# Kernel tuning notes

Measured on AMD Instinct MI355X. Metric: run time of the kernel, lower is better.

## Reference

```python
import jax, jax.numpy as jnp
import numpy as np

IN_FEATURES = 4096
OUT_FEATURES = 11008
GROUP_SIZE = 128


def setup_inputs() -> dict:
    key = jax.random.key(0)
    k_x, k_w, k_s, k_z, k_b = jax.random.split(key, 5)
    x = jax.random.normal(k_x, (8, IN_FEATURES), dtype=jnp.float32)
    # packed INT4 weights: two 4-bit values per byte, stored in int32 (0..255)
    weight_q = jax.random.randint(k_w, (OUT_FEATURES, IN_FEATURES // 2), 0, 256, dtype=jnp.int32)
    num_groups = IN_FEATURES // GROUP_SIZE  # 32
    scales = jax.random.uniform(k_s, (OUT_FEATURES, num_groups), dtype=jnp.float32) * 0.01 + 1e-4
    zeros = jax.random.normal(k_z, (OUT_FEATURES, num_groups), dtype=jnp.float32) * 0.05
    bias = jax.random.normal(k_b, (OUT_FEATURES,), dtype=jnp.float32) * 0.02
    return {"x": x, "weight_q": weight_q, "scales": scales, "zeros": zeros, "bias": bias}


def _dequantize(weight_q, scales, zeros):
    # unpack INT4: low nibble first, then high nibble (matches torch stack order)
    low = weight_q & 15
    high = (weight_q >> 4) & 15
    q = jnp.stack([low, high], axis=-1).reshape(OUT_FEATURES, -1)  # [out, in]
    q = q.astype(scales.dtype)
    num_groups = scales.shape[1]
    q = q[:, : num_groups * GROUP_SIZE].reshape(OUT_FEATURES, num_groups, GROUP_SIZE)
    w = q * scales[:, :, None] + zeros[:, :, None]
    return w.reshape(OUT_FEATURES, -1)[:, :IN_FEATURES]


def reference(x, weight_q, scales, zeros, bias):
    w = _dequantize(weight_q, scales, zeros)            # [out, in]
    return x.astype(w.dtype) @ w.T + bias               # [B, out]
```

## Files before the change

### kernel.cpp

```cpp
#include <hip/hip_runtime.h>

typedef _Float16 f16;
typedef __attribute__((ext_vector_type(2))) _Float16 f16x2;
typedef __attribute__((ext_vector_type(4))) _Float16 f16x4;
typedef __attribute__((ext_vector_type(8))) _Float16 f16x8;
typedef __attribute__((ext_vector_type(4))) float f32x4;
typedef __attribute__((ext_vector_type(4))) unsigned u32x4;

constexpr int IN_F  = 4096;
constexpr int OUT_F = 11008;
constexpr int NGRP  = 32;

__global__ void xprep_kernel(const float* __restrict__ x, f16* __restrict__ xh) {
    int i = (blockIdx.x * blockDim.x + threadIdx.x) * 4;
    float4 v = *(const float4*)(x + i);
    f16x4 r = {(f16)v.x, (f16)v.y, (f16)v.z, (f16)v.w};
    *(f16x4*)(xh + i) = r;
}

__device__ __forceinline__ unsigned dq2(unsigned q, f16x2 sp, f16x2 zp) {
    unsigned t = (((q << 12) | q) & 0x000F000Fu) | 0x64006400u;
    f16x2 u = __builtin_bit_cast(f16x2, t);
    u = u - (f16x2){(_Float16)1024.0f, (_Float16)1024.0f};
    u = u * sp + zp;
    return __builtin_bit_cast(unsigned, u);
}

__device__ __forceinline__ f16x2 bcast(float v) {
    _Float16 h = (_Float16)v;
    return (f16x2){h, h};
}

template<bool PRE>
__global__ __launch_bounds__(256, 4)
void qlin_kernel(const int* __restrict__ wq,
                 const float* __restrict__ scales,
                 const float* __restrict__ zeros,
                 const float* __restrict__ bias,
                 const float* __restrict__ xf,
                 const f16* __restrict__ xh,
                 float* __restrict__ out)
{
    __shared__ f32x4 red[4][64];
    const int tid  = threadIdx.x;
    const int wv   = tid >> 6;
    const int lane = tid & 63;
    const int col  = lane & 15;
    const int kg   = lane >> 4;
    const int o0   = blockIdx.x * 16;
    const int orow = o0 + col;
    const bool mvalid = (col < 8);

    const int kbase = wv * 1024;
    const int g0    = kbase >> 7;

    float4 sa = *(const float4*)(scales + (size_t)orow * NGRP + g0);
    float4 sb = *(const float4*)(scales + (size_t)orow * NGRP + g0 + 4);
    float4 za = *(const float4*)(zeros  + (size_t)orow * NGRP + g0);
    float4 zb = *(const float4*)(zeros  + (size_t)orow * NGRP + g0 + 4);
    f16x2 sp[8] = {bcast(sa.x), bcast(sa.y), bcast(sa.z), bcast(sa.w),
                   bcast(sb.x), bcast(sb.y), bcast(sb.z), bcast(sb.w)};
    f16x2 zp[8] = {bcast(za.x), bcast(za.y), bcast(za.z), bcast(za.w),
                   bcast(zb.x), bcast(zb.y), bcast(zb.z), bcast(zb.w)};

    const int*   wbase = wq + (size_t)orow * (IN_F / 2) + (kbase >> 1) + kg * 4;
    const f16*   xrow  = xh + (size_t)col * IN_F + kbase + kg * 8;
    const float* xfrow = xf + (size_t)col * IN_F + kbase + kg * 8;

    f32x4 acc = {0.f, 0.f, 0.f, 0.f};

    int4  qb[2][4];
    f16x8 ab[2][4];

    #pragma unroll
    for (int t = 0; t < 4; ++t) {
        qb[0][t] = *(const int4*)(wbase + t * 16);
        if (mvalid) {
            if constexpr (PRE) {
                ab[0][t] = *(const f16x8*)(xrow + t * 32);
            } else {
                float4 a0 = *(const float4*)(xfrow + t * 32);
                float4 a1 = *(const float4*)(xfrow + t * 32 + 4);
                ab[0][t] = (f16x8){(f16)a0.x,(f16)a0.y,(f16)a0.z,(f16)a0.w,
                                   (f16)a1.x,(f16)a1.y,(f16)a1.z,(f16)a1.w};
            }
        } else {
            ab[0][t] = (f16x8){0,0,0,0,0,0,0,0};
        }
    }

    #pragma unroll
    for (int gl = 0; gl < 8; ++gl) {
        const int cur = gl & 1, nxt = cur ^ 1;
        if (gl < 7) {
            #pragma unroll
            for (int t = 0; t < 4; ++t) {
                qb[nxt][t] = *(const int4*)(wbase + (gl + 1) * 64 + t * 16);
                if (mvalid) {
                    if constexpr (PRE) {
                        ab[nxt][t] = *(const f16x8*)(xrow + (gl + 1) * 128 + t * 32);
                    } else {
                        float4 a0 = *(const float4*)(xfrow + (gl + 1) * 128 + t * 32);
                        float4 a1 = *(const float4*)(xfrow + (gl + 1) * 128 + t * 32 + 4);
                        ab[nxt][t] = (f16x8){(f16)a0.x,(f16)a0.y,(f16)a0.z,(f16)a0.w,
                                             (f16)a1.x,(f16)a1.y,(f16)a1.z,(f16)a1.w};
                    }
                } else {
                    ab[nxt][t] = (f16x8){0,0,0,0,0,0,0,0};
                }
            }
        }
        const f16x2 s2 = sp[gl], z2 = zp[gl];
        #pragma unroll
        for (int t = 0; t < 4; ++t) {
            const int4 q = qb[cur][t];
            u32x4 bw = {dq2((unsigned)q.x, s2, z2),
                        dq2((unsigned)q.y, s2, z2),
                        dq2((unsigned)q.z, s2, z2),
                        dq2((unsigned)q.w, s2, z2)};
            f16x8 bfr = __builtin_bit_cast(f16x8, bw);
            acc = __builtin_amdgcn_mfma_f32_16x16x32_f16(ab[cur][t], bfr, acc, 0, 0, 0);
        }
    }

    red[wv][lane] = acc;
    __syncthreads();

    if (tid < 64) {
        f32x4 ssum = red[0][tid];
        #pragma unroll
        for (int w = 1; w < 4; ++w) ssum += red[w][tid];
        const int n = tid & 15;
        const float bb = bias[o0 + n];
        const int mbase = (tid >> 4) * 4;
        if (mbase < 8) {
            #pragma unroll
            for (int i = 0; i < 4; ++i)
                out[(size_t)(mbase + i) * OUT_F + o0 + n] = ssum[i] + bb;
        }
    }
}

extern "C" void kernel_launch(void* const* d_in, const int* in_sizes, int n_in,
                              void* d_out, int out_size, void* d_ws, size_t ws_size,
                              hipStream_t stream) {
    const float* x  = (const float*)d_in[0];
    const int*   wq = (const int*)d_in[1];
    const float* sc = (const float*)d_in[2];
    const float* zr = (const float*)d_in[3];
    const float* bs = (const float*)d_in[4];
    float* out = (float*)d_out;

    if (ws_size >= (size_t)(8 * IN_F * sizeof(f16))) {
        f16* xh = (f16*)d_ws;
        xprep_kernel<<<(8 * IN_F) / (256 * 4), 256, 0, stream>>>(x, xh);
        qlin_kernel<true><<<OUT_F / 16, 256, 0, stream>>>(wq, sc, zr, bs, x, xh, out);
    } else {
        qlin_kernel<false><<<OUT_F / 16, 256, 0, stream>>>(wq, sc, zr, bs, x, (const f16*)d_ws, out);
    }
}
```

Measured before the change: 31.11 us.

## Stage INT4 weight tiles into LDS via direct global-to-LDS async loads

Replaces per-lane register prefetch of packed weights with a double-buffered LDS staging scheme that uses global_load_lds, where each wave loads whole contiguous 1 KB row slices with an XOR swizzle. It also re-partitions K so that waves interleave over 128-element chunks within each 512-wide stage, and loads scales and zeros as scalar gathers. The aim is fully coalesced weight streaming and better latency hiding. In exchange it adds 32 KB of LDS per block, which limits occupancy, and a __syncthreads per stage.

```diff
diff --git a/kernel.cpp b/kernel.cpp
--- a/kernel.cpp
+++ b/kernel.cpp
@@ -41,7 +41,9 @@
                  const f16* __restrict__ xh,
                  float* __restrict__ out)
 {
+    __shared__ unsigned char wlds[2][16][1024];
     __shared__ f32x4 red[4][64];
+
     const int tid  = threadIdx.x;
     const int wv   = tid >> 6;
     const int lane = tid & 63;
@@ -51,76 +53,75 @@
     const int orow = o0 + col;
     const bool mvalid = (col < 8);
 
-    const int kbase = wv * 1024;
-    const int g0    = kbase >> 7;
+    f16x2 sp[8], zp[8];
+    #pragma unroll
+    for (int s = 0; s < 8; ++s) {
+        sp[s] = bcast(scales[(size_t)orow * NGRP + s * 4 + wv]);
+        zp[s] = bcast(zeros [(size_t)orow * NGRP + s * 4 + wv]);
+    }
 
-    float4 sa = *(const float4*)(scales + (size_t)orow * NGRP + g0);
-    float4 sb = *(const float4*)(scales + (size_t)orow * NGRP + g0 + 4);
-    float4 za = *(const float4*)(zeros  + (size_t)orow * NGRP + g0);
-    float4 zb = *(const float4*)(zeros  + (size_t)orow * NGRP + g0 + 4);
-    f16x2 sp[8] = {bcast(sa.x), bcast(sa.y), bcast(sa.z), bcast(sa.w),
-                   bcast(sb.x), bcast(sb.y), bcast(sb.z), bcast(sb.w)};
-    f16x2 zp[8] = {bcast(za.x), bcast(za.y), bcast(za.z), bcast(za.w),
-                   bcast(zb.x), bcast(zb.y), bcast(zb.z), bcast(zb.w)};
+    const char* wtile = (const char*)wq + (size_t)o0 * 8192;
 
-    const int*   wbase = wq + (size_t)orow * (IN_F / 2) + (kbase >> 1) + kg * 4;
-    const f16*   xrow  = xh + (size_t)col * IN_F + kbase + kg * 8;
-    const float* xfrow = xf + (size_t)col * IN_F + kbase + kg * 8;
+    auto stage = [&](int sl, int bufi) {
+        #pragma unroll
+        for (int c = 0; c < 4; ++c) {
+            const int r = 4 * wv + c;
+            const char* src = wtile + (size_t)r * 8192 + sl * 1024
+                              + ((lane * 16) ^ ((r & 7) << 4));
+            __builtin_amdgcn_global_load_lds(
+                (const __attribute__((address_space(1))) void*)src,
+                (__attribute__((address_space(3))) void*)&wlds[bufi][r][0],
+                16, 0, 0);
+        }
+    };
+
+    stage(0, 0);
+
+    const f16*   xcol  = xh + (size_t)col * IN_F;
+    const float* xfcol = xf + (size_t)col * IN_F;
+    const unsigned swz = (unsigned)((col & 7) << 4);
 
     f32x4 acc = {0.f, 0.f, 0.f, 0.f};
 
-    int4  qb[2][4];
-    f16x8 ab[2][4];
+    __syncthreads();
 
     #pragma unroll
-    for (int t = 0; t < 4; ++t) {
-        qb[0][t] = *(const int4*)(wbase + t * 16);
-        if (mvalid) {
-            if constexpr (PRE) {
-                ab[0][t] = *(const f16x8*)(xrow + t * 32);
+    for (int s = 0; s < 8; ++s) {
+        const int cur = s & 1;
+        if (s < 7) stage(s + 1, cur ^ 1);
+
+        f16x8 af[4];
+        #pragma unroll
+        for (int t = 0; t < 4; ++t) {
+            const int k = s * 512 + wv * 128 + t * 32 + kg * 8;
+            if (mvalid) {
+                if constexpr (PRE) {
+                    af[t] = *(const f16x8*)(xcol + k);
+                } else {
+                    float4 a0 = *(const float4*)(xfcol + k);
+                    float4 a1 = *(const float4*)(xfcol + k + 4);
+                    af[t] = (f16x8){(f16)a0.x,(f16)a0.y,(f16)a0.z,(f16)a0.w,
+                                    (f16)a1.x,(f16)a1.y,(f16)a1.z,(f16)a1.w};
+                }
             } else {
-                float4 a0 = *(const float4*)(xfrow + t * 32);
-                float4 a1 = *(const float4*)(xfrow + t * 32 + 4);
-                ab[0][t] = (f16x8){(f16)a0.x,(f16)a0.y,(f16)a0.z,(f16)a0.w,
-                                   (f16)a1.x,(f16)a1.y,(f16)a1.z,(f16)a1.w};
-            }
-        } else {
-            ab[0][t] = (f16x8){0,0,0,0,0,0,0,0};
-        }
-    }
-
-    #pragma unroll
-    for (int gl = 0; gl < 8; ++gl) {
-        const int cur = gl & 1, nxt = cur ^ 1;
-        if (gl < 7) {
-            #pragma unroll
-            for (int t = 0; t < 4; ++t) {
-                qb[nxt][t] = *(const int4*)(wbase + (gl + 1) * 64 + t * 16);
-                if (mvalid) {
-                    if constexpr (PRE) {
-                        ab[nxt][t] = *(const f16x8*)(xrow + (gl + 1) * 128 + t * 32);
-                    } else {
-                        float4 a0 = *(const float4*)(xfrow + (gl + 1) * 128 + t * 32);
-                        float4 a1 = *(const float4*)(xfrow + (gl + 1) * 128 + t * 32 + 4);
-                        ab[nxt][t] = (f16x8){(f16)a0.x,(f16)a0.y,(f16)a0.z,(f16)a0.w,
-                                             (f16)a1.x,(f16)a1.y,(f16)a1.z,(f16)a1.w};
-                    }
-                } else {
-                    ab[nxt][t] = (f16x8){0,0,0,0,0,0,0,0};
-                }
+                af[t] = (f16x8){0,0,0,0,0,0,0,0};
             }
         }
-        const f16x2 s2 = sp[gl], z2 = zp[gl];
+
+        const f16x2 s2 = sp[s], z2 = zp[s];
         #pragma unroll
         for (int t = 0; t < 4; ++t) {
-            const int4 q = qb[cur][t];
+            const unsigned off = ((unsigned)(wv * 256 + t * 64 + kg * 16)) ^ swz;
+            const int4 q = *(const int4*)&wlds[cur][col][off];
             u32x4 bw = {dq2((unsigned)q.x, s2, z2),
                         dq2((unsigned)q.y, s2, z2),
                         dq2((unsigned)q.z, s2, z2),
                         dq2((unsigned)q.w, s2, z2)};
             f16x8 bfr = __builtin_bit_cast(f16x8, bw);
-            acc = __builtin_amdgcn_mfma_f32_16x16x32_f16(ab[cur][t], bfr, acc, 0, 0, 0);
+            acc = __builtin_amdgcn_mfma_f32_16x16x32_f16(af[t], bfr, acc, 0, 0, 0);
         }
+
+        __syncthreads();
     }
 
     red[wv][lane] = acc;
```

New measurement: 30.42 us. 1.02x faster.
